# Kernel tuning notes

Hardware: AMD Instinct MI355X
Metric: run time of the kernel (lower is better)

## Reference

```python
import jax, jax.numpy as jnp
import numpy as np

G, N, E = 64, 1000, 8192          # graphs, nodes/graph, edges/graph
F_IN, C, H, HID, NCLS = 128, 128, 4, 256, 2
EPS = 1e-5


def _gcn(x, src, dst, W, b):
    # GCNConv: symmetric normalization with self-loops, sum aggregation.
    h = x @ W                                              # [N, C]
    deg = jax.ops.segment_sum(jnp.ones(E, h.dtype), dst, num_segments=N) + 1.0
    dinv = jax.lax.rsqrt(deg)                              # deg^{-1/2}
    msg = h[src] * (dinv[src] * dinv[dst])[:, None]        # [E, C] gather
    out = jax.ops.segment_sum(msg, dst, num_segments=N)    # scatter-add
    out = out + h * (dinv * dinv)[:, None]                 # self-loop term
    return out + b


def _layernorm(y, g, b):
    mu = y.mean(-1, keepdims=True)
    var = ((y - mu) ** 2).mean(-1, keepdims=True)
    return (y - mu) * jax.lax.rsqrt(var + EPS) * g + b


def setup_inputs() -> dict:
    key = jax.random.key(0)
    ks = jax.random.split(key, 12)
    rn = lambda k, s: jax.random.normal(k, s, jnp.float32) * 0.05
    return dict(
        x=jax.random.normal(ks[0], (G, N, F_IN), jnp.float32),
        edge_index=jax.random.randint(ks[1], (G, 2, E), 0, N),
        W0=rn(ks[2], (F_IN, C)), b0=jnp.zeros((C,), jnp.float32),
        W1=rn(ks[3], (C, C)), b1=jnp.zeros((C,), jnp.float32),
        in_w=rn(ks[4], (3 * C, C)), in_b=jnp.zeros((3 * C,), jnp.float32),
        out_w=rn(ks[5], (C, C)), out_b=jnp.zeros((C,), jnp.float32),
        ln2_g=jnp.ones((C,), jnp.float32), ln2_b=jnp.zeros((C,), jnp.float32),
        mw1=rn(ks[6], (C, HID)), mb1=jnp.zeros((HID,), jnp.float32),
        mw2=rn(ks[7], (HID, C)), mb2=jnp.zeros((C,), jnp.float32),
        lw=rn(ks[8], (C, NCLS)), lb=jnp.zeros((NCLS,), jnp.float32),
    )


def reference(x, edge_index, W0, b0, W1, b1, in_w, in_b, out_w, out_b,
              ln2_g, ln2_b, mw1, mb1, mw2, mb2, lw, lb):
    src, dst = edge_index[:, 0, :], edge_index[:, 1, :]
    conv = jax.vmap(_gcn, in_axes=(0, 0, 0, None, None))
    h = jnp.tanh(conv(x, src, dst, W0, b0))   # [G, N, C]
    h = jnp.tanh(conv(h, src, dst, W1, b1))
    g = h.sum(axis=1)                          # SumAggregation -> [G, C]

    # MultiheadAttention, unbatched: sequence of G graph embeddings
    qkv = g @ in_w.T + in_b
    q, k, v = jnp.split(qkv, 3, axis=-1)
    d = C // H
    qh, kh, vh = (t.reshape(G, H, d) for t in (q, k, v))
    attn = jax.nn.softmax(jnp.einsum('qhd,khd->hqk', qh, kh) * (d ** -0.5), axis=-1)
    o = jnp.einsum('hqk,khd->qhd', attn, vh).reshape(G, C) @ out_w.T + out_b

    x_attend = o                               # dropout = identity (eval)
    # NOTE: original computes layer_norm1(x_attend) but immediately overwrites it.
    mlp = jnp.maximum(x_attend @ mw1 + mb1, 0.0) @ mw2 + mb2
    y = _layernorm(x_attend + mlp, ln2_g, ln2_b)
    node_repr = jnp.maximum(y, 0.0).sum(axis=0)  # [C]
    return node_repr @ lw + lb                   # [NCLS]
```

## Files before the change

### kernel.cpp

```cpp
#include <hip/hip_runtime.h>
#include <math.h>

#define Gn 64
#define Nn 1000
#define En 8192
#define Cc 128
#define HIDn 256
#define EPSf 1e-5f

typedef __attribute__((ext_vector_type(8))) short bh8;
typedef __attribute__((ext_vector_type(4))) float fx4;

__device__ __forceinline__ unsigned short f2bf(float f) {
    unsigned u = __float_as_uint(f);
    u += 0x7fffu + ((u >> 16) & 1u);
    return (unsigned short)(u >> 16);
}
__device__ __forceinline__ float bflo(unsigned u) { return __uint_as_float(u << 16); }
__device__ __forceinline__ float bfhi(unsigned u) { return __uint_as_float(u & 0xffff0000u); }

__global__ __launch_bounds__(1024) void k_pg0(const int* __restrict__ ei, const float* __restrict__ X,
                                              const float* __restrict__ W, int4* __restrict__ ninfo,
                                              int2* __restrict__ epair, float* __restrict__ pooled,
                                              float* __restrict__ repr, int* __restrict__ ctr,
                                              unsigned short* __restrict__ Hout)
{
    __shared__ int degs[1024];
    __shared__ int sb[1024];
    __shared__ int cur[1024];
    __shared__ float dinv_s[1024];
    __shared__ __align__(16) short Wt[128][136];
    int t = threadIdx.x;

    if (blockIdx.x < 64) {
        int g = blockIdx.x;
        const int* srcp = ei + (size_t)g * 2 * En;
        const int* dstp = srcp + En;
        degs[t] = 0;
        __syncthreads();
        for (int e = t; e < En; e += 1024) atomicAdd(&degs[dstp[e]], 1);
        __syncthreads();
        int d = (t < Nn) ? degs[t] : 0;
        sb[t] = d;
        __syncthreads();
        for (int st = 1; st < 1024; st <<= 1) {
            int v2 = (t >= st) ? sb[t - st] : 0;
            __syncthreads();
            sb[t] += v2;
            __syncthreads();
        }
        int ex = sb[t] - d;
        float dv = rsqrtf((float)d + 1.0f);
        cur[t] = ex;
        dinv_s[t] = dv;
        if (t < Nn) ninfo[g * Nn + t] = make_int4(ex, d, __float_as_int(dv * dv), 0);
        __syncthreads();
        for (int e = t; e < En; e += 1024) {
            int dd = dstp[e], ss = srcp[e];
            int p = atomicAdd(&cur[dd], 1);
            float w = dinv_s[ss] * dinv_s[dd];
            epair[(size_t)g * En + p] = make_int2(ss, __float_as_int(w));
        }
        if (t < Cc) pooled[g * Cc + t] = 0.f;
        if (g == 0 && t < Cc) repr[t] = 0.f;
        if (g == 0 && t == 0) *ctr = 0;
    } else {
        int g = blockIdx.x - 64;
        for (int idx = t; idx < 16384; idx += 1024) {
            int kI = idx >> 7, n = idx & 127;
            Wt[n][kI] = (short)f2bf(W[idx]);
        }
        __syncthreads();
        int wave = t >> 6, l = t & 63;
        int lr = l & 15, lg = l >> 4;
        const float* Xf = X + (size_t)g * Nn * Cc;
        unsigned short* Hg = Hout + (size_t)g * Nn * Cc;

        #pragma unroll
        for (int s = 0; s < 4; ++s) {
            int rbase = wave * 64 + s * 16;
            int r = rbase + lr;
            bool ok = r < Nn;
            bh8 af[4];
            #pragma unroll
            for (int ks = 0; ks < 4; ++ks) {
                if (ok) {
                    const float* xp = Xf + (size_t)r * Cc + ks * 32 + lg * 8;
                    fx4 a0 = *(const fx4*)xp;
                    fx4 a1 = *(const fx4*)(xp + 4);
                    bh8 av;
                    av[0] = (short)f2bf(a0[0]); av[1] = (short)f2bf(a0[1]);
                    av[2] = (short)f2bf(a0[2]); av[3] = (short)f2bf(a0[3]);
                    av[4] = (short)f2bf(a1[0]); av[5] = (short)f2bf(a1[1]);
                    av[6] = (short)f2bf(a1[2]); av[7] = (short)f2bf(a1[3]);
                    af[ks] = av;
                } else af[ks] = bh8{0, 0, 0, 0, 0, 0, 0, 0};
            }
            fx4 acc[8];
            #pragma unroll
            for (int ct = 0; ct < 8; ++ct) acc[ct] = fx4{0.f, 0.f, 0.f, 0.f};
            #pragma unroll
            for (int ks = 0; ks < 4; ++ks) {
                #pragma unroll
                for (int ct = 0; ct < 8; ++ct) {
                    bh8 bfr = *(const bh8*)(&Wt[ct * 16 + lr][ks * 32 + lg * 8]);
                    acc[ct] = __builtin_amdgcn_mfma_f32_16x16x32_bf16(af[ks], bfr, acc[ct], 0, 0, 0);
                }
            }
            #pragma unroll
            for (int ct = 0; ct < 8; ++ct) {
                #pragma unroll
                for (int rg = 0; rg < 4; ++rg) {
                    int row = rbase + lg * 4 + rg;
                    if (row < Nn) Hg[(size_t)row * Cc + ct * 16 + lr] = f2bf(acc[ct][rg]);
                }
            }
        }
    }
}

__global__ __launch_bounds__(256) void k_gemm1(const unsigned short* __restrict__ Xh,
                                               const float* __restrict__ W,
                                               unsigned short* __restrict__ Hout)
{
    __shared__ __align__(16) short Wt[128][136];
    int b = blockIdx.x;
    int xcd = b & 7, j = b >> 3;
    int g = xcd + 8 * (j & 7);
    int rblk = j >> 3;
    int t = threadIdx.x;
    for (int idx = t; idx < 16384; idx += 256) {
        int kI = idx >> 7, n = idx & 127;
        Wt[n][kI] = (short)f2bf(W[idx]);
    }
    __syncthreads();
    int wave = t >> 6, l = t & 63;
    int lr = l & 15, lg = l >> 4;
    const short* Xg = (const short*)Xh + (size_t)g * Nn * Cc;
    unsigned short* Hg = Hout + (size_t)g * Nn * Cc;

    for (int s = 0; s < 4; ++s) {
        int rbase = rblk * 256 + wave * 64 + s * 16;
        int r = rbase + lr;
        bool ok = r < Nn;
        bh8 af[4];
        #pragma unroll
        for (int ks = 0; ks < 4; ++ks) {
            if (ok) af[ks] = *(const bh8*)(Xg + (size_t)r * Cc + ks * 32 + lg * 8);
            else    af[ks] = bh8{0, 0, 0, 0, 0, 0, 0, 0};
        }
        fx4 acc[8];
        #pragma unroll
        for (int ct = 0; ct < 8; ++ct) acc[ct] = fx4{0.f, 0.f, 0.f, 0.f};
        #pragma unroll
        for (int ks = 0; ks < 4; ++ks) {
            #pragma unroll
            for (int ct = 0; ct < 8; ++ct) {
                bh8 bfr = *(const bh8*)(&Wt[ct * 16 + lr][ks * 32 + lg * 8]);
                acc[ct] = __builtin_amdgcn_mfma_f32_16x16x32_bf16(af[ks], bfr, acc[ct], 0, 0, 0);
            }
        }
        #pragma unroll
        for (int ct = 0; ct < 8; ++ct) {
            #pragma unroll
            for (int rg = 0; rg < 4; ++rg) {
                int row = rbase + lg * 4 + rg;
                if (row < Nn) Hg[(size_t)row * Cc + ct * 16 + lr] = f2bf(acc[ct][rg]);
            }
        }
    }
}

template<int POOL>
__global__ __launch_bounds__(256) void k_combine(const unsigned* __restrict__ Hb, const int2* __restrict__ epair,
                                                 const int4* __restrict__ ninfo, const float* __restrict__ bias,
                                                 unsigned* __restrict__ Tout, float* __restrict__ pooled)
{
    int b = blockIdx.x;
    int xcd = b & 7, j = b >> 3;
    int g = xcd + 8 * (j & 7);
    int blk = j >> 3;
    int wave = threadIdx.x >> 6, lane = threadIdx.x & 63;
    const unsigned* Hg = Hb + (size_t)g * Nn * 64;
    const int2* epg = epair + (size_t)g * En;
    const int4* nig = ninfo + (size_t)g * Nn;
    float2 bb = *(const float2*)(bias + lane * 2);
    float px = 0.f, py = 0.f;
    for (int n = blk * 4 + wave; n < Nn; n += 128) {
        int4 ni = nig[n];
        int st = ni.x, dc = ni.y;
        float sw = __int_as_float(ni.z);
        unsigned hv = Hg[n * 64 + lane];
        float a0x = bflo(hv) * sw + bb.x, a0y = bfhi(hv) * sw + bb.y;
        float a1x = 0.f, a1y = 0.f, a2x = 0.f, a2y = 0.f, a3x = 0.f, a3y = 0.f;
        int e = 0;
        for (; e + 4 <= dc; e += 4) {
            int2 p0 = epg[st + e];
            int2 p1 = epg[st + e + 1];
            int2 p2 = epg[st + e + 2];
            int2 p3 = epg[st + e + 3];
            unsigned r0 = Hg[p0.x * 64 + lane];
            unsigned r1 = Hg[p1.x * 64 + lane];
            unsigned r2 = Hg[p2.x * 64 + lane];
            unsigned r3 = Hg[p3.x * 64 + lane];
            float w0 = __int_as_float(p0.y), w1 = __int_as_float(p1.y);
            float w2 = __int_as_float(p2.y), w3 = __int_as_float(p3.y);
            a0x = fmaf(bflo(r0), w0, a0x); a0y = fmaf(bfhi(r0), w0, a0y);
            a1x = fmaf(bflo(r1), w1, a1x); a1y = fmaf(bfhi(r1), w1, a1y);
            a2x = fmaf(bflo(r2), w2, a2x); a2y = fmaf(bfhi(r2), w2, a2y);
            a3x = fmaf(bflo(r3), w3, a3x); a3y = fmaf(bfhi(r3), w3, a3y);
        }
        for (; e < dc; ++e) {
            int2 p0 = epg[st + e];
            unsigned r0 = Hg[p0.x * 64 + lane];
            float w0 = __int_as_float(p0.y);
            a0x = fmaf(bflo(r0), w0, a0x); a0y = fmaf(bfhi(r0), w0, a0y);
        }
        float ax = (a0x + a1x) + (a2x + a3x);
        float ay = (a0y + a1y) + (a2y + a3y);
        float tx = tanhf(ax), ty = tanhf(ay);
        if (POOL) { px += tx; py += ty; }
        else Tout[(size_t)(g * Nn + n) * 64 + lane] = ((unsigned)f2bf(ty) << 16) | (unsigned)f2bf(tx);
    }
    if (POOL) {
        atomicAdd(&pooled[g * Cc + lane * 2], px);
        atomicAdd(&pooled[g * Cc + lane * 2 + 1], py);
    }
}

__global__ __launch_bounds__(1024) void k_qkv(const float* __restrict__ pooled, const float* __restrict__ in_w,
                                              const float* __restrict__ in_b, float* __restrict__ qkvb)
{
    int t = threadIdx.x, lane = t & 63, wv = t >> 6;
    int c = blockIdx.x * 16 + wv;
    const float* wr = in_w + c * Cc;
    float w0 = wr[lane], w1 = wr[64 + lane];
    float bias = in_b[c];
    for (int i = 0; i < Gn; ++i) {
        float p = fmaf(pooled[i * Cc + lane], w0, pooled[i * Cc + 64 + lane] * w1);
        #pragma unroll
        for (int off2 = 32; off2 > 0; off2 >>= 1) p += __shfl_xor(p, off2);
        if (lane == 0) qkvb[i * 384 + c] = p + bias;
    }
}

__global__ __launch_bounds__(1024) void k_attn(const float* __restrict__ qkvb, float* __restrict__ ob)
{
    __shared__ float q[64][33], kk[64][33], v[64][33];
    __shared__ float S[64][64];
    int h = blockIdx.x, t = threadIdx.x;

    for (int idx = t; idx < 2048; idx += 1024) {
        int i = idx >> 5, cc = idx & 31;
        q[i][cc]  = qkvb[i * 384 + h * 32 + cc];
        kk[i][cc] = qkvb[i * 384 + 128 + h * 32 + cc];
        v[i][cc]  = qkvb[i * 384 + 256 + h * 32 + cc];
    }
    __syncthreads();

    for (int idx = t; idx < 4096; idx += 1024) {
        int i = idx >> 6, jj = idx & 63;
        float acc = 0.f;
        #pragma unroll
        for (int d2 = 0; d2 < 32; ++d2) acc = fmaf(q[i][d2], kk[jj][d2], acc);
        S[i][jj] = acc * 0.17677669529663687f;
    }
    __syncthreads();

    int lane = t & 63, w = t >> 6;
    for (int r = w; r < 64; r += 16) {
        float val = S[r][lane];
        float m = val;
        #pragma unroll
        for (int off = 32; off > 0; off >>= 1) m = fmaxf(m, __shfl_xor(m, off));
        float e2 = expf(val - m);
        float ssum = e2;
        #pragma unroll
        for (int off = 32; off > 0; off >>= 1) ssum += __shfl_xor(ssum, off);
        S[r][lane] = e2 / ssum;
    }
    __syncthreads();

    for (int idx = t; idx < 2048; idx += 1024) {
        int i = idx >> 5, d2 = idx & 31;
        float acc = 0.f;
        #pragma unroll 4
        for (int k2 = 0; k2 < 64; ++k2) acc = fmaf(S[i][k2], v[k2][d2], acc);
        ob[i * Cc + h * 32 + d2] = acc;
    }
}

__global__ __launch_bounds__(1024) void k_tailfinal(const float* __restrict__ ob, const float* __restrict__ out_w,
                                                    const float* __restrict__ out_b, const float* __restrict__ mw1,
                                                    const float* __restrict__ mb1, const float* __restrict__ mw2,
                                                    const float* __restrict__ mb2, const float* __restrict__ ln2g,
                                                    const float* __restrict__ ln2b, const float* __restrict__ lw,
                                                    const float* __restrict__ lb, float* __restrict__ repr,
                                                    int* __restrict__ ctr, float* __restrict__ out)
{
    __shared__ float sob[4][128];
    __shared__ float sxatt[4][128];
    __shared__ float sm1[4][256];
    __shared__ float spart[4][128];
    __shared__ float pr[128];
    __shared__ int slast;
    int g0 = blockIdx.x * 4;
    int t = threadIdx.x, lane = t & 63, wv = t >> 6;

    if (t < 512) sob[t >> 7][t & 127] = ob[(size_t)(g0 + (t >> 7)) * Cc + (t & 127)];
    if (t < 128) pr[t] = 0.f;
    __syncthreads();

    for (int c = wv; c < Cc; c += 16) {
        float w0 = out_w[c * Cc + lane];
        float w1 = out_w[c * Cc + 64 + lane];
        float bc = out_b[c];
        #pragma unroll
        for (int g = 0; g < 4; ++g) {
            float p = fmaf(sob[g][lane], w0, sob[g][64 + lane] * w1);
            #pragma unroll
            for (int off = 32; off > 0; off >>= 1) p += __shfl_xor(p, off);
            if (lane == 0) sxatt[g][c] = p + bc;
        }
    }
    __syncthreads();

    {
        int j = t & 255, gi = t >> 8;
        float acc = mb1[j];
        #pragma unroll 8
        for (int k = 0; k < Cc; ++k) acc = fmaf(sxatt[gi][k], mw1[k * HIDn + j], acc);
        sm1[gi][j] = fmaxf(acc, 0.f);
    }
    __syncthreads();

    {
        int c = t & 127, gi = (t >> 7) & 3, half = t >> 9;
        int k0 = half * 128;
        float acc = 0.f;
        #pragma unroll 8
        for (int k = 0; k < 128; ++k) acc = fmaf(sm1[gi][k0 + k], mw2[(k0 + k) * Cc + c], acc);
        if (half) spart[gi][c] = acc;
        __syncthreads();
        if (!half) sxatt[gi][c] = sxatt[gi][c] + acc + spart[gi][c] + mb2[c];
    }
    __syncthreads();

    if (t < 256) {
        int g = wv;
        float v0 = sxatt[g][lane], v1 = sxatt[g][64 + lane];
        float s = v0 + v1;
        #pragma unroll
        for (int off = 32; off > 0; off >>= 1) s += __shfl_xor(s, off);
        float mu = s * (1.f / 128.f);
        float d0 = v0 - mu, d1 = v1 - mu;
        float vv = d0 * d0 + d1 * d1;
        #pragma unroll
        for (int off = 32; off > 0; off >>= 1) vv += __shfl_xor(vv, off);
        float rstd = rsqrtf(vv * (1.f / 128.f) + EPSf);
        float z0 = fmaxf(d0 * rstd * ln2g[lane] + ln2b[lane], 0.f);
        float z1 = fmaxf(d1 * rstd * ln2g[64 + lane] + ln2b[64 + lane], 0.f);
        atomicAdd(&pr[lane], z0);
        atomicAdd(&pr[64 + lane], z1);
    }
    __syncthreads();
    if (t < 128) atomicAdd(&repr[t], pr[t]);

    __threadfence();
    __syncthreads();
    if (t == 0) slast = atomicAdd(ctr, 1);
    __syncthreads();
    if (slast == 15) {
        __threadfence();
        __shared__ float r0s[128], r1s[128];
        if (t < 128) {
            float r = __hip_atomic_load(&repr[t], __ATOMIC_RELAXED, __HIP_MEMORY_SCOPE_AGENT);
            r0s[t] = r * lw[t * 2 + 0];
            r1s[t] = r * lw[t * 2 + 1];
        }
        __syncthreads();
        for (int s2 = 64; s2 > 0; s2 >>= 1) {
            if (t < s2) { r0s[t] += r0s[t + s2]; r1s[t] += r1s[t + s2]; }
            __syncthreads();
        }
        if (t == 0) { out[0] = r0s[0] + lb[0]; out[1] = r1s[0] + lb[1]; }
    }
}

extern "C" void kernel_launch(void* const* d_in, const int* in_sizes, int n_in,
                              void* d_out, int out_size, void* d_ws, size_t ws_size,
                              hipStream_t stream)
{
    const float* x     = (const float*)d_in[0];
    const int*   ei    = (const int*)d_in[1];
    const float* W0    = (const float*)d_in[2];
    const float* b0    = (const float*)d_in[3];
    const float* W1    = (const float*)d_in[4];
    const float* b1    = (const float*)d_in[5];
    const float* in_w  = (const float*)d_in[6];
    const float* in_b  = (const float*)d_in[7];
    const float* out_w = (const float*)d_in[8];
    const float* out_b = (const float*)d_in[9];
    const float* ln2g  = (const float*)d_in[10];
    const float* ln2b  = (const float*)d_in[11];
    const float* mw1   = (const float*)d_in[12];
    const float* mb1   = (const float*)d_in[13];
    const float* mw2   = (const float*)d_in[14];
    const float* mb2   = (const float*)d_in[15];
    const float* lw    = (const float*)d_in[16];
    const float* lb    = (const float*)d_in[17];
    float* out = (float*)d_out;
    (void)in_sizes; (void)n_in; (void)out_size; (void)ws_size;

    char* ws = (char*)d_ws;
    size_t off = 0;
    auto carve = [&](size_t bytes) { size_t o = off; off += (bytes + 255) & ~(size_t)255; return o; };
    size_t o_ni    = carve((size_t)Gn * Nn * 16);
    size_t o_ep    = carve((size_t)Gn * En * 8);
    size_t o_pool  = carve((size_t)Gn * Cc * 4);
    size_t o_qkv   = carve((size_t)Gn * 384 * 4);
    size_t o_ob    = carve((size_t)Gn * Cc * 4);
    size_t o_repr  = carve((size_t)Cc * 4);
    size_t o_ctr   = carve(256);
    size_t o_H     = carve((size_t)Gn * Nn * Cc * 2);
    size_t o_T     = carve((size_t)Gn * Nn * Cc * 2);

    int4*  ninfo  = (int4*)(ws + o_ni);
    int2*  epair  = (int2*)(ws + o_ep);
    float* pooled = (float*)(ws + o_pool);
    float* qkvb   = (float*)(ws + o_qkv);
    float* ob     = (float*)(ws + o_ob);
    float* repr   = (float*)(ws + o_repr);
    int*   ctr    = (int*)(ws + o_ctr);
    unsigned short* H = (unsigned short*)(ws + o_H);
    unsigned short* T = (unsigned short*)(ws + o_T);

    k_pg0<<<128, 1024, 0, stream>>>(ei, x, W0, ninfo, epair, pooled, repr, ctr, H);
    k_combine<0><<<2048, 256, 0, stream>>>((const unsigned*)H, epair, ninfo, b0, (unsigned*)T, nullptr);
    k_gemm1<<<256, 256, 0, stream>>>(T, W1, H);
    k_combine<1><<<2048, 256, 0, stream>>>((const unsigned*)H, epair, ninfo, b1, nullptr, pooled);
    k_qkv<<<24, 1024, 0, stream>>>(pooled, in_w, in_b, qkvb);
    k_attn<<<4, 1024, 0, stream>>>(qkvb, ob);
    k_tailfinal<<<16, 1024, 0, stream>>>(ob, out_w, out_b, mw1, mb1, mw2, mb2, ln2g, ln2b,
                                         lw, lb, repr, ctr, out);
}
```

Baseline: 182.5 us.

## Split first-layer GEMM and CSR build into finer 256-thread blocks

Replaces the 128-block, 1024-thread first kernel with 320 blocks of 256 threads. 256 blocks do the X@W0 bf16 MFMA GEMM, each covering a quarter of a graph's rows and using the XCD-aware mapping from k_gemm1. The other 64 blocks build the CSR, now with a wave-shuffle prefix scan over 4 nodes per thread instead of a 10-step barrier scan. The aim is more parallel blocks and fewer barriers on the critical path. The cost is that each GEMM block rebuilds the transposed W tile in shared memory, giving more redundant conversion work.

```diff
diff --git a/kernel.cpp b/kernel.cpp
--- a/kernel.cpp
+++ b/kernel.cpp
@@ -19,101 +19,118 @@
 __device__ __forceinline__ float bflo(unsigned u) { return __uint_as_float(u << 16); }
 __device__ __forceinline__ float bfhi(unsigned u) { return __uint_as_float(u & 0xffff0000u); }
 
-__global__ __launch_bounds__(1024) void k_pg0(const int* __restrict__ ei, const float* __restrict__ X,
-                                              const float* __restrict__ W, int4* __restrict__ ninfo,
-                                              int2* __restrict__ epair, float* __restrict__ pooled,
-                                              float* __restrict__ repr, int* __restrict__ ctr,
-                                              unsigned short* __restrict__ Hout)
-{
-    __shared__ int degs[1024];
-    __shared__ int sb[1024];
-    __shared__ int cur[1024];
+__global__ __launch_bounds__(256) void k_fused(const int* __restrict__ ei, const float* __restrict__ X,
+                                               const float* __restrict__ W, int4* __restrict__ ninfo,
+                                               int2* __restrict__ epair, float* __restrict__ pooled,
+                                               float* __restrict__ repr, int* __restrict__ ctr,
+                                               unsigned short* __restrict__ Hout)
+{
+    __shared__ __align__(16) short Wt[128][136];
+    __shared__ int   curs[1024];
     __shared__ float dinv_s[1024];
-    __shared__ __align__(16) short Wt[128][136];
+    __shared__ int   wsum[4];
     int t = threadIdx.x;
 
-    if (blockIdx.x < 64) {
-        int g = blockIdx.x;
+    if (blockIdx.x >= 256) {
+        int g = blockIdx.x - 256;
         const int* srcp = ei + (size_t)g * 2 * En;
         const int* dstp = srcp + En;
-        degs[t] = 0;
-        __syncthreads();
-        for (int e = t; e < En; e += 1024) atomicAdd(&degs[dstp[e]], 1);
-        __syncthreads();
-        int d = (t < Nn) ? degs[t] : 0;
-        sb[t] = d;
-        __syncthreads();
-        for (int st = 1; st < 1024; st <<= 1) {
-            int v2 = (t >= st) ? sb[t - st] : 0;
-            __syncthreads();
-            sb[t] += v2;
-            __syncthreads();
-        }
-        int ex = sb[t] - d;
-        float dv = rsqrtf((float)d + 1.0f);
-        cur[t] = ex;
-        dinv_s[t] = dv;
-        if (t < Nn) ninfo[g * Nn + t] = make_int4(ex, d, __float_as_int(dv * dv), 0);
-        __syncthreads();
-        for (int e = t; e < En; e += 1024) {
+        int lane = t & 63, wv = t >> 6;
+
+        #pragma unroll
+        for (int j = 0; j < 4; ++j) curs[t * 4 + j] = 0;
+        __syncthreads();
+        for (int e = t; e < En; e += 256) atomicAdd(&curs[dstp[e]], 1);
+        __syncthreads();
+
+        int base = t * 4;
+        int d0 = curs[base], d1 = curs[base + 1], d2 = curs[base + 2], d3 = curs[base + 3];
+        int s = d0 + d1 + d2 + d3;
+        int v = s;
+        #pragma unroll
+        for (int off = 1; off <= 32; off <<= 1) {
+            int u = __shfl_up(v, off);
+            if (lane >= off) v += u;
+        }
+        if (lane == 63) wsum[wv] = v;
+        __syncthreads();
+        int woff = 0;
+        #pragma unroll
+        for (int w = 0; w < 4; ++w) if (w < wv) woff += wsum[w];
+        int e0 = woff + v - s;
+        int e1 = e0 + d0, e2 = e1 + d1, e3 = e2 + d2;
+        float dv0 = rsqrtf((float)d0 + 1.f), dv1 = rsqrtf((float)d1 + 1.f);
+        float dv2 = rsqrtf((float)d2 + 1.f), dv3 = rsqrtf((float)d3 + 1.f);
+        curs[base] = e0; curs[base + 1] = e1; curs[base + 2] = e2; curs[base + 3] = e3;
+        dinv_s[base] = dv0; dinv_s[base + 1] = dv1; dinv_s[base + 2] = dv2; dinv_s[base + 3] = dv3;
+        if (base < Nn)     ninfo[g * Nn + base]     = make_int4(e0, d0, __float_as_int(dv0 * dv0), 0);
+        if (base + 1 < Nn) ninfo[g * Nn + base + 1] = make_int4(e1, d1, __float_as_int(dv1 * dv1), 0);
+        if (base + 2 < Nn) ninfo[g * Nn + base + 2] = make_int4(e2, d2, __float_as_int(dv2 * dv2), 0);
+        if (base + 3 < Nn) ninfo[g * Nn + base + 3] = make_int4(e3, d3, __float_as_int(dv3 * dv3), 0);
+        __syncthreads();
+
+        for (int e = t; e < En; e += 256) {
             int dd = dstp[e], ss = srcp[e];
-            int p = atomicAdd(&cur[dd], 1);
+            int p = atomicAdd(&curs[dd], 1);
             float w = dinv_s[ss] * dinv_s[dd];
             epair[(size_t)g * En + p] = make_int2(ss, __float_as_int(w));
         }
         if (t < Cc) pooled[g * Cc + t] = 0.f;
         if (g == 0 && t < Cc) repr[t] = 0.f;
         if (g == 0 && t == 0) *ctr = 0;
-    } else {
-        int g = blockIdx.x - 64;
-        for (int idx = t; idx < 16384; idx += 1024) {
-            int kI = idx >> 7, n = idx & 127;
-            Wt[n][kI] = (short)f2bf(W[idx]);
-        }
-        __syncthreads();
-        int wave = t >> 6, l = t & 63;
-        int lr = l & 15, lg = l >> 4;
-        const float* Xf = X + (size_t)g * Nn * Cc;
-        unsigned short* Hg = Hout + (size_t)g * Nn * Cc;
-
-        #pragma unroll
-        for (int s = 0; s < 4; ++s) {
-            int rbase = wave * 64 + s * 16;
-            int r = rbase + lr;
-            bool ok = r < Nn;
-            bh8 af[4];
-            #pragma unroll
-            for (int ks = 0; ks < 4; ++ks) {
-                if (ok) {
-                    const float* xp = Xf + (size_t)r * Cc + ks * 32 + lg * 8;
-                    fx4 a0 = *(const fx4*)xp;
-                    fx4 a1 = *(const fx4*)(xp + 4);
-                    bh8 av;
-                    av[0] = (short)f2bf(a0[0]); av[1] = (short)f2bf(a0[1]);
-                    av[2] = (short)f2bf(a0[2]); av[3] = (short)f2bf(a0[3]);
-                    av[4] = (short)f2bf(a1[0]); av[5] = (short)f2bf(a1[1]);
-                    av[6] = (short)f2bf(a1[2]); av[7] = (short)f2bf(a1[3]);
-                    af[ks] = av;
-                } else af[ks] = bh8{0, 0, 0, 0, 0, 0, 0, 0};
-            }
-            fx4 acc[8];
-            #pragma unroll
-            for (int ct = 0; ct < 8; ++ct) acc[ct] = fx4{0.f, 0.f, 0.f, 0.f};
-            #pragma unroll
-            for (int ks = 0; ks < 4; ++ks) {
-                #pragma unroll
-                for (int ct = 0; ct < 8; ++ct) {
-                    bh8 bfr = *(const bh8*)(&Wt[ct * 16 + lr][ks * 32 + lg * 8]);
-                    acc[ct] = __builtin_amdgcn_mfma_f32_16x16x32_bf16(af[ks], bfr, acc[ct], 0, 0, 0);
-                }
-            }
+        return;
+    }
+
+    int b = blockIdx.x;
+    int xcd = b & 7, j = b >> 3;
+    int g = xcd + 8 * (j & 7);
+    int rblk = j >> 3;
+    for (int idx = t; idx < 16384; idx += 256) {
+        int kI = idx >> 7, n = idx & 127;
+        Wt[n][kI] = (short)f2bf(W[idx]);
+    }
+    __syncthreads();
+    int wave = t >> 6, l = t & 63;
+    int lr = l & 15, lg = l >> 4;
+    const float* Xf = X + (size_t)g * Nn * Cc;
+    unsigned short* Hg = Hout + (size_t)g * Nn * Cc;
+
+    for (int s = 0; s < 4; ++s) {
+        int rbase = rblk * 256 + wave * 64 + s * 16;
+        int r = rbase + lr;
+        bool ok = r < Nn;
+        bh8 af[4];
+        #pragma unroll
+        for (int ks = 0; ks < 4; ++ks) {
+            if (ok) {
+                const float* xp = Xf + (size_t)r * Cc + ks * 32 + lg * 8;
+                fx4 a0 = *(const fx4*)xp;
+                fx4 a1 = *(const fx4*)(xp + 4);
+                bh8 av;
+                av[0] = (short)f2bf(a0[0]); av[1] = (short)f2bf(a0[1]);
+                av[2] = (short)f2bf(a0[2]); av[3] = (short)f2bf(a0[3]);
+                av[4] = (short)f2bf(a1[0]); av[5] = (short)f2bf(a1[1]);
+                av[6] = (short)f2bf(a1[2]); av[7] = (short)f2bf(a1[3]);
+                af[ks] = av;
+            } else af[ks] = bh8{0, 0, 0, 0, 0, 0, 0, 0};
+        }
+        fx4 acc[8];
+        #pragma unroll
+        for (int ct = 0; ct < 8; ++ct) acc[ct] = fx4{0.f, 0.f, 0.f, 0.f};
+        #pragma unroll
+        for (int ks = 0; ks < 4; ++ks) {
             #pragma unroll
             for (int ct = 0; ct < 8; ++ct) {
-                #pragma unroll
-                for (int rg = 0; rg < 4; ++rg) {
-                    int row = rbase + lg * 4 + rg;
-                    if (row < Nn) Hg[(size_t)row * Cc + ct * 16 + lr] = f2bf(acc[ct][rg]);
-                }
+                bh8 bfr = *(const bh8*)(&Wt[ct * 16 + lr][ks * 32 + lg * 8]);
+                acc[ct] = __builtin_amdgcn_mfma_f32_16x16x32_bf16(af[ks], bfr, acc[ct], 0, 0, 0);
+            }
+        }
+        #pragma unroll
+        for (int ct = 0; ct < 8; ++ct) {
+            #pragma unroll
+            for (int rg = 0; rg < 4; ++rg) {
+                int row = rbase + lg * 4 + rg;
+                if (row < Nn) Hg[(size_t)row * Cc + ct * 16 + lr] = f2bf(acc[ct][rg]);
             }
         }
     }
@@ -435,7 +452,7 @@
     unsigned short* H = (unsigned short*)(ws + o_H);
     unsigned short* T = (unsigned short*)(ws + o_T);
 
-    k_pg0<<<128, 1024, 0, stream>>>(ei, x, W0, ninfo, epair, pooled, repr, ctr, H);
+    k_fused<<<320, 256, 0, stream>>>(ei, x, W0, ninfo, epair, pooled, repr, ctr, H);
     k_combine<0><<<2048, 256, 0, stream>>>((const unsigned*)H, epair, ninfo, b0, (unsigned*)T, nullptr);
     k_gemm1<<<256, 256, 0, stream>>>(T, W1, H);
     k_combine<1><<<2048, 256, 0, stream>>>((const unsigned*)H, epair, ninfo, b1, nullptr, pooled);
```

Result: faster. 171.9 us (-5.8%).
